# Performance work log

Hardware: AMD Instinct MI355X
Metric: run time of the kernel (lower is better)

## Reference

```python
import jax, jax.numpy as jnp
import numpy as np

HIDDEN = 1024
NUM_TOTAL = 8
NUM_SHARED = 2
NUM_ROUTED = NUM_TOTAL - NUM_SHARED
TOP_K = 2
TOKENS = 16384
SCALE = 0.02


def setup_inputs() -> dict:
    key = jax.random.key(0)
    ks = jax.random.split(key, 12)
    h = HIDDEN
    inp = {
        "x": jax.random.normal(ks[0], (TOKENS, h), dtype=jnp.float32),
        # shared experts: [E_s, in, hidden] / [E_s, hidden] etc. (y = x @ W + b)
        "shared_w1": jax.random.normal(ks[1], (NUM_SHARED, h, h), jnp.float32) * SCALE,
        "shared_b1": jnp.zeros((NUM_SHARED, h), jnp.float32),
        "shared_w2": jax.random.normal(ks[2], (NUM_SHARED, h, h), jnp.float32) * SCALE,
        "shared_b2": jnp.zeros((NUM_SHARED, h), jnp.float32),
        # routed experts
        "routed_w1": jax.random.normal(ks[3], (NUM_ROUTED, h, h), jnp.float32) * SCALE,
        "routed_b1": jnp.zeros((NUM_ROUTED, h), jnp.float32),
        "routed_w2": jax.random.normal(ks[4], (NUM_ROUTED, h, h), jnp.float32) * SCALE,
        "routed_b2": jnp.zeros((NUM_ROUTED, h), jnp.float32),
        # router: Linear(hidden, num_routed)
        "router_w": jax.random.normal(ks[5], (h, NUM_ROUTED), jnp.float32) * SCALE,
        "router_b": jnp.zeros((NUM_ROUTED,), jnp.float32),
    }
    return inp


def _expert_all(x, w1, b1, w2, b2):
    # x: [B, H]; w1/w2: [E, H, H]; returns [B, E, H]
    hmid = jnp.tanh(jnp.einsum("bi,eio->beo", x, w1) + b1)
    return jnp.einsum("beh,eho->beo", hmid, w2) + b2


def reference(x, shared_w1, shared_b1, shared_w2, shared_b2,
              routed_w1, routed_b1, routed_w2, routed_b2,
              router_w, router_b):
    # shared experts: every token through every shared expert, summed
    shared_out = _expert_all(x, shared_w1, shared_b1, shared_w2, shared_b2).sum(axis=1)  # [B,H]

    # router softmax + top-k mask (original weights each expert by
    # routing_weights[:, i] * mask[:, i], i.e. NOT renormalized)
    logits = x @ router_w + router_b                       # [B, E_r]
    routing_weights = jax.nn.softmax(logits, axis=-1)      # [B, E_r]
    _, top_idx = jax.lax.top_k(routing_weights, TOP_K)     # [B, k]
    mask = jax.nn.one_hot(top_idx, NUM_ROUTED, dtype=routing_weights.dtype).sum(axis=1)  # [B, E_r]
    weight = routing_weights * mask                        # [B, E_r]

    # dense all-expert compute masked by top-k (faithful to source loop)
    expert_out = _expert_all(x, routed_w1, routed_b1, routed_w2, routed_b2)  # [B, E_r, H]
    routed_out = jnp.einsum("be,beh->bh", weight, expert_out)

    return shared_out + routed_out
```

## Files before the change

### kernel.cpp

```cpp
#include <hip/hip_runtime.h>
#include <hip/hip_bf16.h>

#define H 1024
#define B_TOK 16384
#define RTILES 262
#define RCAP   (RTILES * 128)

typedef __attribute__((ext_vector_type(8))) short s16x8;
typedef __attribute__((ext_vector_type(4))) float f32x4;

__device__ __forceinline__ short f2bf(float f) {
  __hip_bfloat16 h = __float2bfloat16(f);
  return __builtin_bit_cast(short, h);
}
__device__ __forceinline__ float bf2f(short s) {
  __hip_bfloat16 h = __builtin_bit_cast(__hip_bfloat16, s);
  return __bfloat162float(h);
}

__device__ __forceinline__ float fast_tanh(float x) {
  const float e = __expf(2.f * x);
  return 1.f - __fdividef(2.f, e + 1.f);
}

__device__ __forceinline__ void load_lds16(const short* g, short* l) {
  __builtin_amdgcn_global_load_lds((const __attribute__((address_space(1))) void*)g,
                                   (__attribute__((address_space(3))) void*)l,
                                   16, 0, 0);
}

__global__ void cvt_x_k(const float* __restrict__ x, short* __restrict__ xb) {
  const size_t i = ((size_t)blockIdx.x * blockDim.x + threadIdx.x) * 8;
  const float4 a = *(const float4*)(x + i);
  const float4 b = *(const float4*)(x + i + 4);
  s16x8 v;
  v[0] = f2bf(a.x); v[1] = f2bf(a.y); v[2] = f2bf(a.z); v[3] = f2bf(a.w);
  v[4] = f2bf(b.x); v[5] = f2bf(b.y); v[6] = f2bf(b.z); v[7] = f2bf(b.w);
  *(s16x8*)(xb + i) = v;
}

__global__ void transpose_k(const float* __restrict__ sw1, const float* __restrict__ rw1,
                            const float* __restrict__ sw2, const float* __restrict__ rw2,
                            short* __restrict__ w1t, short* __restrict__ w2t_sh,
                            short* __restrict__ w2t_r) {
  __shared__ float tile[64][65];
  const int z = blockIdx.z;
  const float* src;
  short* dst;
  int ldd = H, koff = 0;
  if (z < 8) {
    src = (z < 2) ? sw1 + (size_t)z * H * H : rw1 + (size_t)(z - 2) * H * H;
    dst = w1t + (size_t)z * H * H;
  } else if (z < 10) {
    const int e = z - 8;
    src = sw2 + (size_t)e * H * H;
    dst = w2t_sh; ldd = 2048; koff = e * 1024;
  } else {
    const int e = z - 10;
    src = rw2 + (size_t)e * H * H;
    dst = w2t_r + (size_t)e * H * H;
  }
  const int k0 = blockIdx.y * 64, n0 = blockIdx.x * 64;
  const int t = threadIdx.x;
#pragma unroll
  for (int i = 0; i < 4; ++i) {
    const int kk = (t >> 4) + 16 * i;
    const int nn = (t & 15) * 4;
    const float4 v = *(const float4*)(src + (size_t)(k0 + kk) * H + n0 + nn);
    tile[nn + 0][kk] = v.x; tile[nn + 1][kk] = v.y;
    tile[nn + 2][kk] = v.z; tile[nn + 3][kk] = v.w;
  }
  __syncthreads();
  const int nn = t >> 2;
  const int kk = (t & 3) * 16;
  s16x8 o0, o1;
#pragma unroll
  for (int u = 0; u < 8; ++u) {
    o0[u] = f2bf(tile[nn][kk + u]);
    o1[u] = f2bf(tile[nn][kk + 8 + u]);
  }
  short* drow = dst + (size_t)(n0 + nn) * ldd + koff + k0 + kk;
  *(s16x8*)(drow) = o0;
  *(s16x8*)(drow + 8) = o1;
}

__global__ void logits_k(const float* __restrict__ x, const float* __restrict__ rw,
                         const float* __restrict__ rb, int2* __restrict__ tk) {
  const int lane = threadIdx.x & 63;
  const int b = blockIdx.x * 4 + (threadIdx.x >> 6);
  const float* xr = x + (size_t)b * H;
  float p[6] = {0.f, 0.f, 0.f, 0.f, 0.f, 0.f};
  for (int k = lane; k < H; k += 64) {
    const float xv = xr[k];
    const float* r = rw + k * 6;
#pragma unroll
    for (int e = 0; e < 6; ++e) p[e] += xv * r[e];
  }
#pragma unroll
  for (int e = 0; e < 6; ++e) {
    float v = p[e];
    for (int off = 32; off > 0; off >>= 1) v += __shfl_down(v, off);
    p[e] = v;
  }
  if (lane == 0) {
    float lg[6];
    float mx = -1e30f;
#pragma unroll
    for (int e = 0; e < 6; ++e) { lg[e] = p[e] + rb[e]; mx = fmaxf(mx, lg[e]); }
    float s = 0.f;
#pragma unroll
    for (int e = 0; e < 6; ++e) { lg[e] = __expf(lg[e] - mx); s += lg[e]; }
    const float inv = 1.f / s;
#pragma unroll
    for (int e = 0; e < 6; ++e) lg[e] *= inv;
    int i1 = 0;
#pragma unroll
    for (int e = 1; e < 6; ++e) if (lg[e] > lg[i1]) i1 = e;
    int i2 = (i1 == 0) ? 1 : 0;
#pragma unroll
    for (int e = 0; e < 6; ++e) if (e != i1 && lg[e] > lg[i2]) i2 = e;
    int2 v;
    v.x = i1 | ((int)(unsigned short)f2bf(lg[i1]) << 16);
    v.y = i2 | ((int)(unsigned short)f2bf(lg[i2]) << 16);
    tk[b] = v;
  }
}

__global__ void hist_k(const int2* __restrict__ tk, int* __restrict__ g) {
  __shared__ int h[6];
  const int t = threadIdx.x;
  if (t < 6) h[t] = 0;
  __syncthreads();
  const int2 v = tk[blockIdx.x * 256 + t];
  atomicAdd(&h[v.x & 0xffff], 1);
  atomicAdd(&h[v.y & 0xffff], 1);
  __syncthreads();
  if (t < 6) atomicAdd(&g[t], h[t]);
}

__global__ void prefix_k(int* __restrict__ g) {
  if (threadIdx.x == 0) {
    int run = 0;
#pragma unroll
    for (int e = 0; e < 6; ++e) {
      g[8 + e] = run; g[16 + e] = run;
      run += (g[e] + 127) & ~127;
    }
    g[14] = run;
  }
}

__global__ void scatter_k(const int2* __restrict__ tk, int* __restrict__ g,
                          int* __restrict__ asg) {
  __shared__ int lcnt[6];
  __shared__ int lbase[6];
  const int t = threadIdx.x;
  if (t < 6) lcnt[t] = 0;
  __syncthreads();
  const int tok = blockIdx.x * 256 + t;
  const int2 v = tk[tok];
  const int e1 = v.x & 0xffff, e2 = v.y & 0xffff;
  const int p1 = atomicAdd(&lcnt[e1], 1);
  const int p2 = atomicAdd(&lcnt[e2], 1);
  __syncthreads();
  if (t < 6) lbase[t] = atomicAdd(&g[16 + t], lcnt[t]);
  __syncthreads();
  asg[lbase[e1] + p1] = tok | (v.x & 0xffff0000);
  asg[lbase[e2] + p2] = tok | (v.y & 0xffff0000);
}

__device__ __forceinline__ void gemm_core64(const short* __restrict__ A, int lda,
                                            const short* __restrict__ Bt, int ldb, int K,
                                            short* smem, int m0, int n0,
                                            const int* __restrict__ asg, int acap,
                                            f32x4 acc[4][4]) {
  const int tid = threadIdx.x, lane = tid & 63, w = tid >> 6;
  const int q8 = (lane >> 4) * 8, r16 = lane & 15;
  const int wr = w >> 1, wc = w & 1;

  const short* gp[4];
#pragma unroll
  for (int ii = 0; ii < 4; ++ii) {
    const int c2 = w * 4 + ii;
    if (c2 < 8) {
      int slot = m0 + c2 * 16 + r16;
      int gr;
      if (asg) {
        int tv = asg[slot] & 0xffff;
        gr = tv < B_TOK ? tv : B_TOK - 1;
      } else {
        gr = slot < acap ? slot : acap - 1;
      }
      gp[ii] = A + (size_t)gr * lda + q8;
    } else {
      gp[ii] = Bt + (size_t)(n0 + (c2 - 8) * 16 + r16) * ldb + q8;
    }
  }
  short* lw0 = smem + w * 4096;
  short* lw1 = smem + 16384 + w * 4096;

#pragma unroll
  for (int i = 0; i < 8; ++i)
    load_lds16(gp[i >> 1] + (i & 1) * 32, lw0 + i * 512);
#pragma unroll
  for (int i = 0; i < 8; ++i)
    load_lds16(gp[i >> 1] + 64 + (i & 1) * 32, lw1 + i * 512);

  const int nsteps = K >> 6;
  int cur = 0;
  for (int t = 0; t < nsteps; ++t) {
    if (t + 1 < nsteps)
      asm volatile("s_waitcnt vmcnt(8)" ::: "memory");
    else
      asm volatile("s_waitcnt vmcnt(0)" ::: "memory");
    __builtin_amdgcn_sched_barrier(0);
    __builtin_amdgcn_s_barrier();
    const short* lc = cur ? smem + 16384 : smem;
    short* lwn = cur ? lw1 : lw0;

    s16x8 af0[4], bf0[4], af1[4], bf1[4];
#pragma unroll
    for (int i = 0; i < 4; ++i)
      af0[i] = *(const s16x8*)(lc + ((wr * 4 + i) * 2 + 0) * 512 + lane * 8);
#pragma unroll
    for (int j = 0; j < 4; ++j)
      bf0[j] = *(const s16x8*)(lc + (16 + (wc * 4 + j) * 2 + 0) * 512 + lane * 8);
    __builtin_amdgcn_s_setprio(1);
#pragma unroll
    for (int i = 0; i < 4; ++i)
#pragma unroll
      for (int j = 0; j < 4; ++j)
        acc[i][j] = __builtin_amdgcn_mfma_f32_16x16x32_bf16(af0[i], bf0[j], acc[i][j], 0, 0, 0);
    __builtin_amdgcn_s_setprio(0);

#pragma unroll
    for (int i = 0; i < 4; ++i)
      af1[i] = *(const s16x8*)(lc + ((wr * 4 + i) * 2 + 1) * 512 + lane * 8);
#pragma unroll
    for (int j = 0; j < 4; ++j)
      bf1[j] = *(const s16x8*)(lc + (16 + (wc * 4 + j) * 2 + 1) * 512 + lane * 8);
    asm volatile("s_waitcnt lgkmcnt(0)" ::: "memory");
    __builtin_amdgcn_sched_barrier(0);
    __builtin_amdgcn_s_barrier();

    if (t + 2 < nsteps) {
#pragma unroll
      for (int i = 0; i < 8; ++i)
        load_lds16(gp[i >> 1] + (t + 2) * 64 + (i & 1) * 32, lwn + i * 512);
    }
    __builtin_amdgcn_s_setprio(1);
#pragma unroll
    for (int i = 0; i < 4; ++i)
#pragma unroll
      for (int j = 0; j < 4; ++j)
        acc[i][j] = __builtin_amdgcn_mfma_f32_16x16x32_bf16(af1[i], bf1[j], acc[i][j], 0, 0, 0);
    __builtin_amdgcn_s_setprio(0);
    cur ^= 1;
  }
}

template <int ROUTED>
__global__ __launch_bounds__(256) void gemm1_k(const short* __restrict__ A, int lda,
                                               const short* __restrict__ W1, int ldb, int K,
                                               const float* __restrict__ b1,
                                               short* __restrict__ Out, int ldo,
                                               const int* __restrict__ asg,
                                               const int* __restrict__ g, int rowcap) {
  const int m0 = blockIdx.x * 128, n0 = blockIdx.y * 128;
  const short* Bt = W1;
  const float* bias = b1;
  if (ROUTED) {
    if (m0 >= g[14]) return;
    int e = 0;
#pragma unroll
    for (int j = 1; j < 6; ++j) if (m0 >= g[8 + j]) e = j;
    Bt = W1 + (size_t)e * H * H;
    bias = b1 + (size_t)e * H;
  }
  __shared__ __align__(16) short smem[32768];
  f32x4 acc[4][4];
#pragma unroll
  for (int i = 0; i < 4; ++i)
#pragma unroll
    for (int j = 0; j < 4; ++j) acc[i][j] = (f32x4){0.f, 0.f, 0.f, 0.f};
  gemm_core64(A, lda, Bt, ldb, K, smem, m0, n0, ROUTED ? asg : nullptr, 1 << 30, acc);

  const int tid = threadIdx.x, lane = tid & 63, w = tid >> 6;
  const int wr = w >> 1, wc = w & 1, q = lane >> 4, c16 = lane & 15;
  __syncthreads();
#pragma unroll
  for (int j = 0; j < 4; ++j) {
    const int colL = wc * 64 + j * 16 + c16;
    const float bv = bias[n0 + colL];
#pragma unroll
    for (int i = 0; i < 4; ++i)
#pragma unroll
      for (int r = 0; r < 4; ++r)
        smem[(wr * 64 + i * 16 + q * 4 + r) * 128 + colL] = f2bf(fast_tanh(acc[i][j][r] + bv));
  }
  __syncthreads();
#pragma unroll
  for (int p = 0; p < 8; ++p) {
    const int rowL = p * 16 + (tid >> 4);
    const int colL = (tid & 15) * 8;
    const int gr = m0 + rowL;
    if (gr < rowcap)
      *(s16x8*)(Out + (size_t)gr * ldo + n0 + colL) = *(const s16x8*)(smem + rowL * 128 + colL);
  }
}

template <int MODE>
__global__ __launch_bounds__(256) void gemm2_k(const short* __restrict__ A, int lda,
                                               const short* __restrict__ W2, int ldb, int K,
                                               const float* __restrict__ b2a,
                                               const float* __restrict__ b2b,
                                               float* __restrict__ Out,
                                               const int* __restrict__ asg,
                                               const int* __restrict__ g, int acap) {
  const int m0 = blockIdx.x * 128, n0 = blockIdx.y * 128;
  const short* Bt = W2;
  const float* bias = b2a;
  if (MODE == 3) {
    if (m0 >= g[14]) return;
    int e = 0;
#pragma unroll
    for (int j = 1; j < 6; ++j) if (m0 >= g[8 + j]) e = j;
    Bt = W2 + (size_t)e * H * H;
    bias = b2a + (size_t)e * H;
  }
  __shared__ __align__(16) short smem[32768];
  f32x4 acc[4][4];
#pragma unroll
  for (int i = 0; i < 4; ++i)
#pragma unroll
    for (int j = 0; j < 4; ++j) acc[i][j] = (f32x4){0.f, 0.f, 0.f, 0.f};
  gemm_core64(A, lda, Bt, ldb, K, smem, m0, n0, nullptr, acap, acc);

  const int tid = threadIdx.x, lane = tid & 63, w = tid >> 6;
  const int wr = w >> 1, wc = w & 1, q = lane >> 4, c16 = lane & 15;

  if (MODE == 0) {
    float* cs = (float*)smem;
    __syncthreads();
#pragma unroll
    for (int half = 0; half < 2; ++half) {
      if (wr == half) {
#pragma unroll
        for (int j = 0; j < 4; ++j) {
          const int colL = wc * 64 + j * 16 + c16;
          const float bv = b2a[n0 + colL] + b2b[n0 + colL];
#pragma unroll
          for (int i = 0; i < 4; ++i)
#pragma unroll
            for (int r = 0; r < 4; ++r)
              cs[(i * 16 + q * 4 + r) * 128 + colL] = acc[i][j][r] + bv;
        }
      }
      __syncthreads();
#pragma unroll
      for (int p = 0; p < 8; ++p) {
        const int rowL = p * 8 + (tid >> 5);
        const int colL = (tid & 31) * 4;
        *(float4*)(Out + (size_t)(m0 + half * 64 + rowL) * H + n0 + colL) =
            *(const float4*)(cs + rowL * 128 + colL);
      }
      __syncthreads();
    }
  } else {
    const int mb = m0 + wr * 64, nb = n0 + wc * 64;
#pragma unroll
    for (int i = 0; i < 4; ++i) {
      int av[4];
#pragma unroll
      for (int r = 0; r < 4; ++r) av[r] = asg[mb + i * 16 + q * 4 + r];
#pragma unroll
      for (int j = 0; j < 4; ++j) {
        const int col = nb + j * 16 + c16;
        const float bv = bias[col];
#pragma unroll
        for (int r = 0; r < 4; ++r) {
          if (av[r] == -1) continue;
          const int tok = av[r] & 0xffff;
          const float wt = bf2f((short)((unsigned)av[r] >> 16));
          atomicAdd(&Out[(size_t)tok * H + col], (acc[i][j][r] + bv) * wt);
        }
      }
    }
  }
}

extern "C" void kernel_launch(void* const* d_in, const int* in_sizes, int n_in,
                              void* d_out, int out_size, void* d_ws, size_t ws_size,
                              hipStream_t stream) {
  const float* x        = (const float*)d_in[0];
  const float* sw1      = (const float*)d_in[1];
  const float* sb1      = (const float*)d_in[2];
  const float* sw2      = (const float*)d_in[3];
  const float* sb2      = (const float*)d_in[4];
  const float* rw1      = (const float*)d_in[5];
  const float* rb1      = (const float*)d_in[6];
  const float* rw2      = (const float*)d_in[7];
  const float* rb2      = (const float*)d_in[8];
  const float* router_w = (const float*)d_in[9];
  const float* router_b = (const float*)d_in[10];
  float* out = (float*)d_out;

  char* ws = (char*)d_ws;
  short* xb     = (short*)(ws);
  short* w1t    = (short*)(ws + (size_t)33554432);
  short* w2t_r  = (short*)(ws + (size_t)50331648);
  short* w2t_sh = (short*)(ws + (size_t)62914560);
  short* hm_sh  = (short*)(ws + (size_t)67108864);
  short* hm_r   = (short*)(ws + (size_t)62914560);
  int2*  tk     = (int2*)hm_sh;
  int*   g      = (int*)(ws + (size_t)134217728);
  int*   asg    = (int*)(ws + (size_t)134217984);

  hipMemsetAsync(g, 0, 64, stream);
  hipMemsetAsync(asg, 0xFF, RCAP * sizeof(int), stream);

  cvt_x_k<<<8192, 256, 0, stream>>>(x, xb);
  transpose_k<<<dim3(16, 16, 16), 256, 0, stream>>>(sw1, rw1, sw2, rw2, w1t, w2t_sh, w2t_r);
  logits_k<<<4096, 256, 0, stream>>>(x, router_w, router_b, tk);
  hist_k<<<64, 256, 0, stream>>>(tk, g);
  prefix_k<<<1, 64, 0, stream>>>(g);
  scatter_k<<<64, 256, 0, stream>>>(tk, g, asg);

  gemm1_k<0><<<dim3(128, 16), 256, 0, stream>>>(xb, H, w1t, H, H, sb1, hm_sh, 2048,
                                                nullptr, nullptr, 1 << 30);
  gemm2_k<0><<<dim3(128, 8), 256, 0, stream>>>(hm_sh, 2048, w2t_sh, 2048, 2048,
                                               sb2, sb2 + H, out, nullptr, nullptr, 1 << 30);

  gemm1_k<1><<<dim3(RTILES, 8), 256, 0, stream>>>(xb, H, w1t + (size_t)2 * H * H, H, H,
                                                  rb1, hm_r, H, asg, g, RCAP);
  gemm2_k<3><<<dim3(RTILES, 8), 256, 0, stream>>>(hm_r, H, w2t_r, H, H,
                                                  rb2, nullptr, out, asg, g, RCAP);
}
```

Baseline: 791.3 us.

## Enlarge GEMM tiles to 256x256 with 8 waves per block

Moves all four expert GEMMs from 128x128 tiles on 256 threads to 256x256 tiles on 512 threads, doubling LDS staging to 128 KB and giving each wave an 8x4 MFMA accumulator block. Routed expert groups are padded to 256 rows so each tile stays within one expert. The aim is to raise arithmetic intensity and cut global reloads of A and B per FLOP. In exchange there are fewer blocks, so wave quantization across CUs is coarser, register pressure is higher, occupancy is lower, and the larger padding adds wasted rows in the routed GEMMs.

```diff
diff --git a/kernel.cpp b/kernel.cpp
--- a/kernel.cpp
+++ b/kernel.cpp
@@ -3,8 +3,8 @@
 
 #define H 1024
 #define B_TOK 16384
-#define RTILES 262
-#define RCAP   (RTILES * 128)
+#define RTILES 134
+#define RCAP   (RTILES * 256)
 
 typedef __attribute__((ext_vector_type(8))) short s16x8;
 typedef __attribute__((ext_vector_type(4))) float f32x4;
@@ -144,7 +144,7 @@
 #pragma unroll
     for (int e = 0; e < 6; ++e) {
       g[8 + e] = run; g[16 + e] = run;
-      run += (g[e] + 127) & ~127;
+      run += (g[e] + 255) & ~255;
     }
     g[14] = run;
   }
@@ -169,20 +169,20 @@
   asg[lbase[e2] + p2] = tok | (v.y & 0xffff0000);
 }
 
-__device__ __forceinline__ void gemm_core64(const short* __restrict__ A, int lda,
-                                            const short* __restrict__ Bt, int ldb, int K,
-                                            short* smem, int m0, int n0,
-                                            const int* __restrict__ asg, int acap,
-                                            f32x4 acc[4][4]) {
+__device__ __forceinline__ void gemm_core256(const short* __restrict__ A, int lda,
+                                             const short* __restrict__ Bt, int ldb, int K,
+                                             short* smem, int m0, int n0,
+                                             const int* __restrict__ asg, int acap,
+                                             f32x4 acc[8][4]) {
   const int tid = threadIdx.x, lane = tid & 63, w = tid >> 6;
   const int q8 = (lane >> 4) * 8, r16 = lane & 15;
-  const int wr = w >> 1, wc = w & 1;
+  const int wr = w >> 2, wc = w & 3;
 
   const short* gp[4];
 #pragma unroll
   for (int ii = 0; ii < 4; ++ii) {
     const int c2 = w * 4 + ii;
-    if (c2 < 8) {
+    if (c2 < 16) {
       int slot = m0 + c2 * 16 + r16;
       int gr;
       if (asg) {
@@ -193,11 +193,11 @@
       }
       gp[ii] = A + (size_t)gr * lda + q8;
     } else {
-      gp[ii] = Bt + (size_t)(n0 + (c2 - 8) * 16 + r16) * ldb + q8;
+      gp[ii] = Bt + (size_t)(n0 + (c2 - 16) * 16 + r16) * ldb + q8;
     }
   }
   short* lw0 = smem + w * 4096;
-  short* lw1 = smem + 16384 + w * 4096;
+  short* lw1 = smem + 32768 + w * 4096;
 
 #pragma unroll
   for (int i = 0; i < 8; ++i)
@@ -215,30 +215,30 @@
       asm volatile("s_waitcnt vmcnt(0)" ::: "memory");
     __builtin_amdgcn_sched_barrier(0);
     __builtin_amdgcn_s_barrier();
-    const short* lc = cur ? smem + 16384 : smem;
+    const short* lc = cur ? smem + 32768 : smem;
     short* lwn = cur ? lw1 : lw0;
 
-    s16x8 af0[4], bf0[4], af1[4], bf1[4];
-#pragma unroll
-    for (int i = 0; i < 4; ++i)
-      af0[i] = *(const s16x8*)(lc + ((wr * 4 + i) * 2 + 0) * 512 + lane * 8);
+    s16x8 af0[8], bf0[4], af1[8], bf1[4];
+#pragma unroll
+    for (int i = 0; i < 8; ++i)
+      af0[i] = *(const s16x8*)(lc + ((wr * 8 + i) * 2 + 0) * 512 + lane * 8);
 #pragma unroll
     for (int j = 0; j < 4; ++j)
-      bf0[j] = *(const s16x8*)(lc + (16 + (wc * 4 + j) * 2 + 0) * 512 + lane * 8);
+      bf0[j] = *(const s16x8*)(lc + ((16 + wc * 4 + j) * 2 + 0) * 512 + lane * 8);
     __builtin_amdgcn_s_setprio(1);
 #pragma unroll
-    for (int i = 0; i < 4; ++i)
+    for (int i = 0; i < 8; ++i)
 #pragma unroll
       for (int j = 0; j < 4; ++j)
         acc[i][j] = __builtin_amdgcn_mfma_f32_16x16x32_bf16(af0[i], bf0[j], acc[i][j], 0, 0, 0);
     __builtin_amdgcn_s_setprio(0);
 
 #pragma unroll
-    for (int i = 0; i < 4; ++i)
-      af1[i] = *(const s16x8*)(lc + ((wr * 4 + i) * 2 + 1) * 512 + lane * 8);
+    for (int i = 0; i < 8; ++i)
+      af1[i] = *(const s16x8*)(lc + ((wr * 8 + i) * 2 + 1) * 512 + lane * 8);
 #pragma unroll
     for (int j = 0; j < 4; ++j)
-      bf1[j] = *(const s16x8*)(lc + (16 + (wc * 4 + j) * 2 + 1) * 512 + lane * 8);
+      bf1[j] = *(const s16x8*)(lc + ((16 + wc * 4 + j) * 2 + 1) * 512 + lane * 8);
     asm volatile("s_waitcnt lgkmcnt(0)" ::: "memory");
     __builtin_amdgcn_sched_barrier(0);
     __builtin_amdgcn_s_barrier();
@@ -250,7 +250,7 @@
     }
     __builtin_amdgcn_s_setprio(1);
 #pragma unroll
-    for (int i = 0; i < 4; ++i)
+    for (int i = 0; i < 8; ++i)
 #pragma unroll
       for (int j = 0; j < 4; ++j)
         acc[i][j] = __builtin_amdgcn_mfma_f32_16x16x32_bf16(af1[i], bf1[j], acc[i][j], 0, 0, 0);
@@ -260,13 +260,13 @@
 }
 
 template <int ROUTED>
-__global__ __launch_bounds__(256) void gemm1_k(const short* __restrict__ A, int lda,
-                                               const short* __restrict__ W1, int ldb, int K,
-                                               const float* __restrict__ b1,
-                                               short* __restrict__ Out, int ldo,
-                                               const int* __restrict__ asg,
-                                               const int* __restrict__ g, int rowcap) {
-  const int m0 = blockIdx.x * 128, n0 = blockIdx.y * 128;
+__global__ __launch_bounds__(512, 2) void gemm1_k(const short* __restrict__ A, int lda,
+                                                  const short* __restrict__ W1, int ldb, int K,
+                                                  const float* __restrict__ b1,
+                                                  short* __restrict__ Out, int ldo,
+                                                  const int* __restrict__ asg,
+                                                  const int* __restrict__ g, int rowcap) {
+  const int m0 = blockIdx.x * 256, n0 = blockIdx.y * 256;
   const short* Bt = W1;
   const float* bias = b1;
   if (ROUTED) {
@@ -277,47 +277,56 @@
     Bt = W1 + (size_t)e * H * H;
     bias = b1 + (size_t)e * H;
   }
-  __shared__ __align__(16) short smem[32768];
-  f32x4 acc[4][4];
-#pragma unroll
-  for (int i = 0; i < 4; ++i)
+  __shared__ __align__(16) short smem[65536];
+  f32x4 acc[8][4];
+#pragma unroll
+  for (int i = 0; i < 8; ++i)
 #pragma unroll
     for (int j = 0; j < 4; ++j) acc[i][j] = (f32x4){0.f, 0.f, 0.f, 0.f};
-  gemm_core64(A, lda, Bt, ldb, K, smem, m0, n0, ROUTED ? asg : nullptr, 1 << 30, acc);
+  gemm_core256(A, lda, Bt, ldb, K, smem, m0, n0, ROUTED ? asg : nullptr, 1 << 30, acc);
 
   const int tid = threadIdx.x, lane = tid & 63, w = tid >> 6;
-  const int wr = w >> 1, wc = w & 1, q = lane >> 4, c16 = lane & 15;
-  __syncthreads();
-#pragma unroll
-  for (int j = 0; j < 4; ++j) {
-    const int colL = wc * 64 + j * 16 + c16;
-    const float bv = bias[n0 + colL];
-#pragma unroll
-    for (int i = 0; i < 4; ++i)
-#pragma unroll
-      for (int r = 0; r < 4; ++r)
-        smem[(wr * 64 + i * 16 + q * 4 + r) * 128 + colL] = f2bf(fast_tanh(acc[i][j][r] + bv));
-  }
-  __syncthreads();
-#pragma unroll
-  for (int p = 0; p < 8; ++p) {
-    const int rowL = p * 16 + (tid >> 4);
-    const int colL = (tid & 15) * 8;
-    const int gr = m0 + rowL;
-    if (gr < rowcap)
-      *(s16x8*)(Out + (size_t)gr * ldo + n0 + colL) = *(const s16x8*)(smem + rowL * 128 + colL);
+  const int wr = w >> 2, wc = w & 3, q = lane >> 4, c16 = lane & 15;
+  __syncthreads();
+#pragma unroll
+  for (int half = 0; half < 2; ++half) {
+    if (wr == half) {
+#pragma unroll
+      for (int j = 0; j < 4; ++j) {
+        const int colL = wc * 64 + j * 16 + c16;
+        const float bv = bias[n0 + colL];
+#pragma unroll
+        for (int i = 0; i < 8; ++i)
+#pragma unroll
+          for (int r = 0; r < 4; ++r)
+            smem[(i * 16 + q * 4 + r) * 256 + colL] = f2bf(fast_tanh(acc[i][j][r] + bv));
+      }
+    }
+    __syncthreads();
+#pragma unroll
+    for (int p = 0; p < 4; ++p) {
+      const int rowL = p * 32 + (tid >> 4);
+      const int colL = (tid & 15) * 16;
+      const int gr = m0 + half * 128 + rowL;
+      if (gr < rowcap) {
+        *(s16x8*)(Out + (size_t)gr * ldo + n0 + colL) = *(const s16x8*)(smem + rowL * 256 + colL);
+        *(s16x8*)(Out + (size_t)gr * ldo + n0 + colL + 8) =
+            *(const s16x8*)(smem + rowL * 256 + colL + 8);
+      }
+    }
+    __syncthreads();
   }
 }
 
 template <int MODE>
-__global__ __launch_bounds__(256) void gemm2_k(const short* __restrict__ A, int lda,
-                                               const short* __restrict__ W2, int ldb, int K,
-                                               const float* __restrict__ b2a,
-                                               const float* __restrict__ b2b,
-                                               float* __restrict__ Out,
-                                               const int* __restrict__ asg,
-                                               const int* __restrict__ g, int acap) {
-  const int m0 = blockIdx.x * 128, n0 = blockIdx.y * 128;
+__global__ __launch_bounds__(512, 2) void gemm2_k(const short* __restrict__ A, int lda,
+                                                  const short* __restrict__ W2, int ldb, int K,
+                                                  const float* __restrict__ b2a,
+                                                  const float* __restrict__ b2b,
+                                                  float* __restrict__ Out,
+                                                  const int* __restrict__ asg,
+                                                  const int* __restrict__ g, int acap) {
+  const int m0 = blockIdx.x * 256, n0 = blockIdx.y * 256;
   const short* Bt = W2;
   const float* bias = b2a;
   if (MODE == 3) {
@@ -328,16 +337,16 @@
     Bt = W2 + (size_t)e * H * H;
     bias = b2a + (size_t)e * H;
   }
-  __shared__ __align__(16) short smem[32768];
-  f32x4 acc[4][4];
-#pragma unroll
-  for (int i = 0; i < 4; ++i)
+  __shared__ __align__(16) short smem[65536];
+  f32x4 acc[8][4];
+#pragma unroll
+  for (int i = 0; i < 8; ++i)
 #pragma unroll
     for (int j = 0; j < 4; ++j) acc[i][j] = (f32x4){0.f, 0.f, 0.f, 0.f};
-  gemm_core64(A, lda, Bt, ldb, K, smem, m0, n0, nullptr, acap, acc);
+  gemm_core256(A, lda, Bt, ldb, K, smem, m0, n0, nullptr, acap, acc);
 
   const int tid = threadIdx.x, lane = tid & 63, w = tid >> 6;
-  const int wr = w >> 1, wc = w & 1, q = lane >> 4, c16 = lane & 15;
+  const int wr = w >> 2, wc = w & 3, q = lane >> 4, c16 = lane & 15;
 
   if (MODE == 0) {
     float* cs = (float*)smem;
@@ -350,26 +359,27 @@
           const int colL = wc * 64 + j * 16 + c16;
           const float bv = b2a[n0 + colL] + b2b[n0 + colL];
 #pragma unroll
-          for (int i = 0; i < 4; ++i)
+          for (int i = 0; i < 8; ++i)
 #pragma unroll
             for (int r = 0; r < 4; ++r)
-              cs[(i * 16 + q * 4 + r) * 128 + colL] = acc[i][j][r] + bv;
+              cs[(i * 16 + q * 4 + r) * 256 + colL] = acc[i][j][r] + bv;
         }
       }
       __syncthreads();
 #pragma unroll
-      for (int p = 0; p < 8; ++p) {
-        const int rowL = p * 8 + (tid >> 5);
-        const int colL = (tid & 31) * 4;
-        *(float4*)(Out + (size_t)(m0 + half * 64 + rowL) * H + n0 + colL) =
-            *(const float4*)(cs + rowL * 128 + colL);
+      for (int p = 0; p < 16; ++p) {
+        const int idx = p * 512 + tid;
+        const int rowL = idx >> 6;
+        const int colL = (idx & 63) * 4;
+        *(float4*)(Out + (size_t)(m0 + half * 128 + rowL) * H + n0 + colL) =
+            *(const float4*)(cs + rowL * 256 + colL);
       }
       __syncthreads();
     }
   } else {
-    const int mb = m0 + wr * 64, nb = n0 + wc * 64;
-#pragma unroll
-    for (int i = 0; i < 4; ++i) {
+    const int mb = m0 + wr * 128, nb = n0 + wc * 64;
+#pragma unroll
+    for (int i = 0; i < 8; ++i) {
       int av[4];
 #pragma unroll
       for (int r = 0; r < 4; ++r) av[r] = asg[mb + i * 16 + q * 4 + r];
@@ -426,13 +436,13 @@
   prefix_k<<<1, 64, 0, stream>>>(g);
   scatter_k<<<64, 256, 0, stream>>>(tk, g, asg);
 
-  gemm1_k<0><<<dim3(128, 16), 256, 0, stream>>>(xb, H, w1t, H, H, sb1, hm_sh, 2048,
-                                                nullptr, nullptr, 1 << 30);
-  gemm2_k<0><<<dim3(128, 8), 256, 0, stream>>>(hm_sh, 2048, w2t_sh, 2048, 2048,
-                                               sb2, sb2 + H, out, nullptr, nullptr, 1 << 30);
-
-  gemm1_k<1><<<dim3(RTILES, 8), 256, 0, stream>>>(xb, H, w1t + (size_t)2 * H * H, H, H,
+  gemm1_k<0><<<dim3(64, 8), 512, 0, stream>>>(xb, H, w1t, H, H, sb1, hm_sh, 2048,
+                                              nullptr, nullptr, 1 << 30);
+  gemm2_k<0><<<dim3(64, 4), 512, 0, stream>>>(hm_sh, 2048, w2t_sh, 2048, 2048,
+                                              sb2, sb2 + H, out, nullptr, nullptr, 1 << 30);
+
+  gemm1_k<1><<<dim3(RTILES, 4), 512, 0, stream>>>(xb, H, w1t + (size_t)2 * H * H, H, H,
                                                   rb1, hm_r, H, asg, g, RCAP);
-  gemm2_k<3><<<dim3(RTILES, 8), 256, 0, stream>>>(hm_r, H, w2t_r, H, H,
+  gemm2_k<3><<<dim3(RTILES, 4), 512, 0, stream>>>(hm_r, H, w2t_r, H, H,
                                                   rb2, nullptr, out, asg, g, RCAP);
 }
```

Measured after the change: 753.4 us. -4.8%, faster.
